# Performance work log

Hardware: AMD Instinct MI355X
Metric: run time of the kernel (lower is better)

## Reference

```python
import jax, jax.numpy as jnp
import numpy as np

N_HEAD = 16

def setup_inputs() -> dict:
    key = jax.random.key(0)
    ks = jax.random.split(key, 5)
    C = 1024
    s = 1.0 / np.sqrt(C)
    x = jax.random.normal(ks[0], (2, 2048, C), dtype=jnp.float32)
    wq = jax.random.normal(ks[1], (C, C), dtype=jnp.float32) * s
    wk = jax.random.normal(ks[2], (C, C), dtype=jnp.float32) * s
    wv = jax.random.normal(ks[3], (C, C), dtype=jnp.float32) * s
    wp = jax.random.normal(ks[4], (C, C), dtype=jnp.float32) * s
    z = jnp.zeros((C,), dtype=jnp.float32)
    return {"x": x, "wq": wq, "bq": z, "wk": wk, "bk": z,
            "wv": wv, "bv": z, "wp": wp, "bp": z}

def reference(x, wq, bq, wk, bk, wv, bv, wp, bp):
    B, T, C = x.shape
    H = N_HEAD
    D = C // H
    # projections: weights stored as (in, out) -> x @ w + b
    q = (x @ wq + bq).reshape(B, T, H, D).transpose(0, 2, 1, 3)  # [B,H,T,D]
    k = (x @ wk + bk).reshape(B, T, H, D).transpose(0, 2, 1, 3)
    v = (x @ wv + bv).reshape(B, T, H, D).transpose(0, 2, 1, 3)
    att = jnp.einsum('bhqd,bhkd->bhqk', q, k) / jnp.sqrt(jnp.float32(D))
    causal = jnp.tril(jnp.ones((T, T), dtype=bool))
    att = jnp.where(causal[None, None], att, -jnp.inf)
    att = jax.nn.softmax(att, axis=-1)
    out = jnp.einsum('bhqk,bhkd->bhqd', att, v)  # [B,H,T,D]
    out = out.transpose(0, 2, 1, 3).reshape(B, T, C)
    return out @ wp + bp
```

## Files before the change

### kernel.cpp

```cpp
#include <hip/hip_runtime.h>
#include <hip/hip_bf16.h>
#include <stdint.h>


typedef __attribute__((ext_vector_type(8)))  short bf16x8;
typedef __attribute__((ext_vector_type(4)))  float f32x4;
typedef __attribute__((ext_vector_type(16))) float f32x16;
typedef __attribute__((ext_vector_type(4)))  short short4v;

#define MFMA16(a,b,c) __builtin_amdgcn_mfma_f32_16x16x32_bf16(a,b,c,0,0,0)
#define MFMA32(a,b,c) __builtin_amdgcn_mfma_f32_32x32x16_bf16(a,b,c,0,0,0)

__device__ __forceinline__ unsigned short f2bfu(float f){
  union { __hip_bfloat16 h; unsigned short u; } cv;
  cv.h = __float2bfloat16(f);
  return cv.u;
}
__device__ __forceinline__ float bfu2f(unsigned u){
  union { unsigned v; float f; } cv;
  cv.v = u << 16;
  return cv.f;
}

__device__ __forceinline__ unsigned cvtpk(float a, float b){
  unsigned r;
  asm("v_cvt_pk_bf16_f32 %0, %1, %2" : "=v"(r) : "v"(a), "v"(b));
  return r;
}

__device__ __forceinline__ void permswap(unsigned &x, unsigned &y){
  asm volatile("v_permlane32_swap_b32 %0, %1" : "+v"(x), "+v"(y));
}

__device__ __forceinline__ void async16(const void* g, void* s){
  __builtin_amdgcn_global_load_lds((const __attribute__((address_space(1))) void*)g,
                                   (__attribute__((address_space(3))) void*)s, 16, 0, 0);
}

__global__ __launch_bounds__(256)
void prep_k(const float* __restrict__ x, unsigned short* __restrict__ xb,
            const float* __restrict__ wq, const float* __restrict__ wk,
            const float* __restrict__ wv, const float* __restrict__ wp,
            unsigned short* __restrict__ wqkvT, unsigned short* __restrict__ wpT)
{
  __shared__ float t[32][33];
  const int bx = blockIdx.x;
  const int tid = threadIdx.x;
  if (bx < 4096) {
    const int i = bx * 256 + tid;
    const float4 v = ((const float4*)x)[i];
    short4v o;
    o.x = (short)f2bfu(v.x); o.y = (short)f2bfu(v.y);
    o.z = (short)f2bfu(v.z); o.w = (short)f2bfu(v.w);
    ((short4v*)xb)[i] = o;
    return;
  }
  const int b = bx - 4096;
  const int wsel = b >> 10;
  const float* W = (wsel == 0) ? wq : (wsel == 1) ? wk : (wsel == 2) ? wv : wp;
  unsigned short* Wt = (wsel == 3) ? wpT : wqkvT + (size_t)wsel * 1024 * 1024;
  const int bc = ((b & 1023) & 31) * 32;
  const int br = ((b & 1023) >> 5) * 32;
  const int tx = tid & 31, ty = tid >> 5;
  #pragma unroll
  for (int i = 0; i < 32; i += 8)
    t[ty + i][tx] = W[(size_t)(br + ty + i) * 1024 + bc + tx];
  __syncthreads();
  #pragma unroll
  for (int i = 0; i < 32; i += 8)
    Wt[(size_t)(bc + ty + i) * 1024 + br + tx] = f2bfu(t[tx][ty + i]);
}

__global__ __launch_bounds__(256)
void gemm_qkv(const unsigned short* __restrict__ A, const unsigned short* __restrict__ Bt,
              const float* __restrict__ b0, const float* __restrict__ b1, const float* __restrict__ b2,
              unsigned short* __restrict__ Qo, unsigned short* __restrict__ Ko,
              unsigned short* __restrict__ Vo)
{
  constexpr int K = 1024;
  __shared__ unsigned short As[2][128 * 32];
  __shared__ unsigned short Bs[2][128 * 32];
  const int tid = threadIdx.x;
  const int lane = tid & 63;
  const int w = tid >> 6;
  const int l15 = lane & 15, lhi = lane >> 4;
  const int row0 = blockIdx.y * 128;
  const int col0 = blockIdx.x * 128;
  const int wr = (w >> 1) * 64;
  const int wc = (w & 1) * 64;

  f32x4 acc[4][4];
  #pragma unroll
  for (int i = 0; i < 4; i++)
    #pragma unroll
    for (int j = 0; j < 4; j++) acc[i][j] = 0.0f;

  const int srow = lane >> 2;
  const int scol = (lane & 3) * 8;
  const unsigned short* Ab = A  + (size_t)(row0 + w * 32 + srow) * K + scol;
  const unsigned short* Bb = Bt + (size_t)(col0 + w * 32 + srow) * K + scol;
  const int wofs = (w * 32) * 32;

  auto stageg = [&](int k0, int buf) {
    async16(Ab + k0,          &As[buf][wofs]);
    async16(Ab + k0 + 16 * K, &As[buf][wofs + 16 * 32]);
    async16(Bb + k0,          &Bs[buf][wofs]);
    async16(Bb + k0 + 16 * K, &Bs[buf][wofs + 16 * 32]);
  };

  stageg(0, 0);
  __syncthreads();
  int cur = 0;
  for (int k0 = 0; k0 < K; k0 += 32) {
    if (k0 + 32 < K) stageg(k0 + 32, cur ^ 1);
    bf16x8 af[4], bfv[4];
    #pragma unroll
    for (int i = 0; i < 4; i++) {
      af[i]  = *(const bf16x8*)&As[cur][(wr + i * 16 + l15) * 32 + lhi * 8];
      bfv[i] = *(const bf16x8*)&Bs[cur][(wc + i * 16 + l15) * 32 + lhi * 8];
    }
    __builtin_amdgcn_s_setprio(1);
    #pragma unroll
    for (int i = 0; i < 4; i++)
      #pragma unroll
      for (int j = 0; j < 4; j++)
        acc[i][j] = MFMA16(af[i], bfv[j], acc[i][j]);
    __builtin_amdgcn_s_setprio(0);
    __syncthreads();
    cur ^= 1;
  }

  #pragma unroll
  for (int j = 0; j < 4; j++) {
    const int n = col0 + wc + j * 16 + l15;
    const int which = n >> 10;
    const int cn = n & 1023;
    const float bias = (which == 0 ? b0[cn] : which == 1 ? b1[cn] : b2[cn]);
    const int h = cn >> 6, d = cn & 63;
    if (which == 2) {
      #pragma unroll
      for (int i = 0; i < 4; i++) {
        const int m = row0 + wr + i * 16 + lhi * 4;
        const int b_ = m >> 11, t = m & 2047;
        uint2 pk;
        pk.x = cvtpk(acc[i][j][0] + bias, acc[i][j][1] + bias);
        pk.y = cvtpk(acc[i][j][2] + bias, acc[i][j][3] + bias);
        *(uint2*)(Vo + (((size_t)(b_ * 16 + h) * 64 + d) * 2048 + t)) = pk;
      }
    } else {
      unsigned short* dst = (which == 0 ? Qo : Ko);
      const float sc = (which == 0 ? 0.125f * 1.44269504f : 1.0f);
      #pragma unroll
      for (int i = 0; i < 4; i++)
        #pragma unroll
        for (int r = 0; r < 4; r++) {
          const int m = row0 + wr + i * 16 + lhi * 4 + r;
          const int b_ = m >> 11, t = m & 2047;
          dst[(((size_t)(b_ * 16 + h) * 2048 + t) * 64) + d] =
              f2bfu((acc[i][j][r] + bias) * sc);
        }
    }
  }
}

__global__ __launch_bounds__(256)
void gemm_proj(const unsigned short* __restrict__ A, const unsigned short* __restrict__ Bt,
               const float* __restrict__ bias_, float* __restrict__ Fo)
{
  constexpr int K = 1024;
  __shared__ unsigned short As[2][64 * 32];
  __shared__ unsigned short Bs[2][128 * 32];
  const int tid = threadIdx.x;
  const int lane = tid & 63;
  const int w = tid >> 6;
  const int l15 = lane & 15, lhi = lane >> 4;
  const int row0 = blockIdx.y * 64;
  const int col0 = blockIdx.x * 128;
  const int wr = (w >> 1) * 32;
  const int wc = (w & 1) * 64;

  f32x4 acc[2][4];
  #pragma unroll
  for (int i = 0; i < 2; i++)
    #pragma unroll
    for (int j = 0; j < 4; j++) acc[i][j] = 0.0f;

  const int srow = lane >> 2;
  const int scol = (lane & 3) * 8;
  const unsigned short* Ab = A  + (size_t)(row0 + w * 16 + srow) * K + scol;
  const unsigned short* Bb = Bt + (size_t)(col0 + w * 32 + srow) * K + scol;
  const int wofsA = (w * 16) * 32;
  const int wofsB = (w * 32) * 32;

  auto stageg = [&](int k0, int buf) {
    async16(Ab + k0,          &As[buf][wofsA]);
    async16(Bb + k0,          &Bs[buf][wofsB]);
    async16(Bb + k0 + 16 * K, &Bs[buf][wofsB + 16 * 32]);
  };

  stageg(0, 0);
  __syncthreads();
  int cur = 0;
  for (int k0 = 0; k0 < K; k0 += 32) {
    if (k0 + 32 < K) stageg(k0 + 32, cur ^ 1);
    bf16x8 af[2], bfv[4];
    #pragma unroll
    for (int i = 0; i < 2; i++)
      af[i]  = *(const bf16x8*)&As[cur][(wr + i * 16 + l15) * 32 + lhi * 8];
    #pragma unroll
    for (int j = 0; j < 4; j++)
      bfv[j] = *(const bf16x8*)&Bs[cur][(wc + j * 16 + l15) * 32 + lhi * 8];
    __builtin_amdgcn_s_setprio(1);
    #pragma unroll
    for (int i = 0; i < 2; i++)
      #pragma unroll
      for (int j = 0; j < 4; j++)
        acc[i][j] = MFMA16(af[i], bfv[j], acc[i][j]);
    __builtin_amdgcn_s_setprio(0);
    __syncthreads();
    cur ^= 1;
  }

  #pragma unroll
  for (int j = 0; j < 4; j++) {
    const int n = col0 + wc + j * 16 + l15;
    const float bias = bias_[n];
    #pragma unroll
    for (int i = 0; i < 2; i++)
      #pragma unroll
      for (int r = 0; r < 4; r++) {
        const int m = row0 + wr + i * 16 + lhi * 4 + r;
        Fo[(size_t)m * 1024 + n] = acc[i][j][r] + bias;
      }
  }
}


__global__ __launch_bounds__(256)
void attn_k(const unsigned short* __restrict__ Q, const unsigned short* __restrict__ Kg,
            const unsigned short* __restrict__ VT,
            unsigned short* __restrict__ Op0, unsigned short* __restrict__ Op1,
            float* __restrict__ ml0, float* __restrict__ ml1)
{
  __shared__ unsigned short Ks[2][64 * 64];
  __shared__ unsigned short Vs[2][64 * 64];
  const int flat = blockIdx.y * 8 + blockIdx.x;
  const int u = (flat & 7) * 32 + (flat >> 3);
  const int bx = u & 7, bh = u >> 3;
  const int e = blockIdx.z;
  const int tid = threadIdx.x, lane = tid & 63, w = tid >> 6;
  const int r0 = lane & 31, hi5 = lane >> 5;
  const int p  = bx * 4 + w;
  const int pB = 63 - p;
  const int q0A = p * 32, q0B = pB * 32;
  const int jmA = p >> 1, jmB = pB >> 1;
  const int jmax = (63 - bx * 4) >> 1;

  unsigned short* Op = e ? Op1 : Op0;
  float* ml = e ? ml1 : ml0;

  const unsigned short* Kbh  = Kg + (size_t)bh * (2048 * 64);
  const unsigned short* VTbh = VT + (size_t)bh * (64 * 2048);

  bf16x8 qfA[4], qfB[4];
  {
    const unsigned short* QA = Q + ((size_t)bh * 2048 + q0A + r0) * 64 + hi5 * 8;
    const unsigned short* QB = Q + ((size_t)bh * 2048 + q0B + r0) * 64 + hi5 * 8;
    #pragma unroll
    for (int s = 0; s < 4; s++) {
      qfA[s] = *(const bf16x8*)(QA + s * 16);
      qfB[s] = *(const bf16x8*)(QB + s * 16);
    }
  }

  f32x16 oA[2], oB[2];
  #pragma unroll
  for (int d = 0; d < 2; d++) { oA[d] = 0.0f; oB[d] = 0.0f; }
  float mA = -1e30f, lA = 0.0f, mB = -1e30f, lB = 0.0f;

  int fragoff[4];
  #pragma unroll
  for (int t = 0; t < 4; t++)
    fragoff[t] = (r0 * 128 + t * 32 + hi5 * 16) ^ ((r0 & 7) << 4);

  const int srow = w * 8 + (lane >> 3);
  const int cole = (((lane & 7) ^ (lane >> 3)) << 3);
  const unsigned short* Ksrc = Kbh + (size_t)srow * 64 + cole;
  const unsigned short* Vsrc = VTbh + (size_t)srow * 2048 + cole;

  auto stage = [&](int kv0, int buf) {
    unsigned short* kb = &Ks[buf][w * 512];
    unsigned short* vb = &Vs[buf][w * 512];
    #pragma unroll
    for (int it = 0; it < 2; ++it) {
      async16(Ksrc + (size_t)(kv0 + it * 32) * 64, kb + it * 2048);
      async16(Vsrc + (size_t)(it * 32) * 2048 + kv0, vb + it * 2048);
    }
  };

  const unsigned short* Ksb;
  const unsigned short* Vsb;

  auto member = [&](f32x16 (&oT)[2], const bf16x8 (&qf)[4],
                    float& mrun, float& lrun, int q0, int kv0, bool mask) {
    f32x16 s0 = 0.0f, s1 = 0.0f;
    __builtin_amdgcn_s_setprio(1);
    #pragma unroll
    for (int t = 0; t < 4; t++) {
      const bf16x8 ka = *(const bf16x8*)((const char*)Ksb + fragoff[t]);
      const bf16x8 kb = *(const bf16x8*)((const char*)Ksb + fragoff[t] + 4096);
      s0 = MFMA32(ka, qf[t], s0);
      s1 = MFMA32(kb, qf[t], s1);
    }
    __builtin_amdgcn_s_setprio(0);

    const int q = q0 + r0;
    if (mask) {
      #pragma unroll
      for (int r = 0; r < 16; r++) {
        const int kvr = kv0 + (r & 3) + 8 * (r >> 2) + 4 * hi5;
        if (kvr      > q) s0[r] = -1e30f;
        if (kvr + 32 > q) s1[r] = -1e30f;
      }
    }

    float pm = fmaxf(s0[0], s1[0]);
    #pragma unroll
    for (int r = 1; r < 16; r++) pm = fmaxf(pm, fmaxf(s0[r], s1[r]));
    pm = fmaxf(pm, __shfl_xor(pm, 32, 64));

    if (__any((int)(pm > mrun + 8.0f))) {
      const float mnew = fmaxf(mrun, pm);
      const float sc = exp2f(mrun - mnew);
      mrun = mnew; lrun *= sc;
      oT[0] *= sc; oT[1] *= sc;
    }

    float p0[16], p1[16];
    float rs = 0.0f;
    #pragma unroll
    for (int r = 0; r < 16; r++) {
      p0[r] = exp2f(s0[r] - mrun);
      p1[r] = exp2f(s1[r] - mrun);
      rs += p0[r] + p1[r];
    }
    rs += __shfl_xor(rs, 32, 64);
    lrun += rs;

    bf16x8 pb[4];
    #pragma unroll
    for (int sub = 0; sub < 2; sub++) {
      {
        unsigned a = cvtpk(p0[sub*8+0], p0[sub*8+1]);
        unsigned b = cvtpk(p0[sub*8+2], p0[sub*8+3]);
        unsigned c = cvtpk(p0[sub*8+4], p0[sub*8+5]);
        unsigned d = cvtpk(p0[sub*8+6], p0[sub*8+7]);
        permswap(a, c); permswap(b, d);
        union { unsigned u[4]; bf16x8 hv; } wv_;
        wv_.u[0] = a; wv_.u[1] = b; wv_.u[2] = c; wv_.u[3] = d;
        pb[sub] = wv_.hv;
      }
      {
        unsigned a = cvtpk(p1[sub*8+0], p1[sub*8+1]);
        unsigned b = cvtpk(p1[sub*8+2], p1[sub*8+3]);
        unsigned c = cvtpk(p1[sub*8+4], p1[sub*8+5]);
        unsigned d = cvtpk(p1[sub*8+6], p1[sub*8+7]);
        permswap(a, c); permswap(b, d);
        union { unsigned u[4]; bf16x8 hv; } wv_;
        wv_.u[0] = a; wv_.u[1] = b; wv_.u[2] = c; wv_.u[3] = d;
        pb[2 + sub] = wv_.hv;
      }
    }

    __builtin_amdgcn_s_setprio(1);
    #pragma unroll
    for (int t = 0; t < 4; t++) {
      const bf16x8 va = *(const bf16x8*)((const char*)Vsb + fragoff[t]);
      const bf16x8 vb = *(const bf16x8*)((const char*)Vsb + fragoff[t] + 4096);
      oT[0] = MFMA32(va, pb[t], oT[0]);
      oT[1] = MFMA32(vb, pb[t], oT[1]);
    }
    __builtin_amdgcn_s_setprio(0);
  };

  stage(e * 64, 0);
  __syncthreads();

  int cur = 0;
  for (int t = e; t <= jmax; t += 2) {
    if (t + 2 <= jmax) stage((t + 2) * 64, cur ^ 1);
    Ksb = &Ks[cur][0];
    Vsb = &Vs[cur][0];
    const int kv0 = t * 64;
    if (t <= jmB) member(oB, qfB, mB, lB, q0B, kv0, t == jmB);
    if (t <= jmA) member(oA, qfA, mA, lA, q0A, kv0, t == jmA);
    __syncthreads();
    cur ^= 1;
  }

  auto emitp = [&](f32x16 (&oT)[2], float m, float l, int p_) {
    const float inv = (l > 0.0f) ? 1.0f / l : 0.0f;
    const size_t rbase = (size_t)(bh * 64 + p_) * 32 + r0;
    if (hi5 == 0) {
      float2 v; v.x = m; v.y = l;
      *(float2*)(ml + rbase * 2) = v;
    }
    unsigned short* base = Op + rbase * 64 + hi5 * 4;
    #pragma unroll
    for (int dh = 0; dh < 2; dh++)
      #pragma unroll
      for (int g = 0; g < 4; g++) {
        uint2 pk;
        pk.x = cvtpk(oT[dh][4*g]   * inv, oT[dh][4*g+1] * inv);
        pk.y = cvtpk(oT[dh][4*g+2] * inv, oT[dh][4*g+3] * inv);
        *(uint2*)(base + dh * 32 + g * 8) = pk;
      }
  };
  emitp(oA, mA, lA, p);
  emitp(oB, mB, lB, pB);
}

__global__ __launch_bounds__(256)
void combine_k(const unsigned short* __restrict__ O0, const unsigned short* __restrict__ O1,
               const float* __restrict__ ml0, const float* __restrict__ ml1,
               unsigned short* __restrict__ Ob)
{
  const int g = blockIdx.x;
  const int bh = g >> 6, p = g & 63;
  const int b_ = bh >> 4, h = bh & 15;
  const int tid = threadIdx.x;
  const int row = tid >> 3, c8 = (tid & 7) * 8;
  const size_t rbase = (size_t)g * 32 + row;
  const float2 v0 = *(const float2*)(ml0 + rbase * 2);
  const float2 v1 = *(const float2*)(ml1 + rbase * 2);
  const float mm = fmaxf(v0.x, v1.x);
  const float w0 = v0.y * exp2f(v0.x - mm);
  const float w1 = v1.y * exp2f(v1.x - mm);
  const float inv = 1.0f / (w0 + w1);
  const float a0 = w0 * inv, a1 = w1 * inv;
  const uint4 u0 = *(const uint4*)(O0 + rbase * 64 + c8);
  const uint4 u1 = *(const uint4*)(O1 + rbase * 64 + c8);
  uint4 o;
  o.x = cvtpk(a0 * bfu2f(u0.x & 0xffffu) + a1 * bfu2f(u1.x & 0xffffu),
              a0 * bfu2f(u0.x >> 16)     + a1 * bfu2f(u1.x >> 16));
  o.y = cvtpk(a0 * bfu2f(u0.y & 0xffffu) + a1 * bfu2f(u1.y & 0xffffu),
              a0 * bfu2f(u0.y >> 16)     + a1 * bfu2f(u1.y >> 16));
  o.z = cvtpk(a0 * bfu2f(u0.z & 0xffffu) + a1 * bfu2f(u1.z & 0xffffu),
              a0 * bfu2f(u0.z >> 16)     + a1 * bfu2f(u1.z >> 16));
  o.w = cvtpk(a0 * bfu2f(u0.w & 0xffffu) + a1 * bfu2f(u1.w & 0xffffu),
              a0 * bfu2f(u0.w >> 16)     + a1 * bfu2f(u1.w >> 16));
  unsigned short* dst = Ob + ((size_t)b_ * 2048 + p * 32 + row) * 1024 + h * 64 + c8;
  *(uint4*)dst = o;
}


extern "C" void kernel_launch(void* const* d_in, const int* in_sizes, int n_in,
                              void* d_out, int out_size, void* d_ws, size_t ws_size,
                              hipStream_t stream) {
  const float* x  = (const float*)d_in[0];
  const float* wq = (const float*)d_in[1];
  const float* bq = (const float*)d_in[2];
  const float* wk = (const float*)d_in[3];
  const float* bk = (const float*)d_in[4];
  const float* wv = (const float*)d_in[5];
  const float* bv = (const float*)d_in[6];
  const float* wp = (const float*)d_in[7];
  const float* bp = (const float*)d_in[8];
  float* out = (float*)d_out;

  char* ws = (char*)d_ws;
  const size_t MB = 1024 * 1024;
  unsigned short* xb    = (unsigned short*)(ws);
  unsigned short* wqkvT = (unsigned short*)(ws + 8  * MB);
  unsigned short* wpT   = (unsigned short*)(ws + 14 * MB);
  unsigned short* Qb    = (unsigned short*)(ws + 16 * MB);
  unsigned short* Kb    = (unsigned short*)(ws + 24 * MB);
  unsigned short* VTb   = (unsigned short*)(ws + 32 * MB);
  unsigned short* Op0   = (unsigned short*)(ws);
  float*          ml0   = (float*)(ws + 8 * MB);
  float*          ml1   = (float*)(ws + 8 * MB + 512 * 1024);
  unsigned short* Op1   = (unsigned short*)d_out;
  unsigned short* Ob    = Qb;

  prep_k<<<dim3(8192), dim3(256), 0, stream>>>(x, xb, wq, wk, wv, wp, wqkvT, wpT);

  gemm_qkv<<<dim3(24, 32), dim3(256), 0, stream>>>(xb, wqkvT, bq, bk, bv,
                                                   Qb, Kb, VTb);
  attn_k<<<dim3(8, 32, 2), dim3(256), 0, stream>>>(Qb, Kb, VTb, Op0, Op1, ml0, ml1);
  combine_k<<<dim3(2048), dim3(256), 0, stream>>>(Op0, Op1, ml0, ml1, Ob);
  gemm_proj<<<dim3(8, 64), dim3(256), 0, stream>>>(Ob, wpT, bp, out);
}
```

Measured before the change: 122.7 us.

## Fuse split-KV attention combine into output projection GEMM A-tile load

```diff
diff --git a/kernel.cpp b/kernel.cpp
--- a/kernel.cpp
+++ b/kernel.cpp
@@ -235,6 +235,115 @@
   }
 }
 
+__global__ __launch_bounds__(256)
+void gemm_projf(const unsigned short* __restrict__ O0, const unsigned short* __restrict__ O1,
+                const float* __restrict__ ml0, const float* __restrict__ ml1,
+                const unsigned short* __restrict__ Bt,
+                const float* __restrict__ bias_, float* __restrict__ Fo)
+{
+  constexpr int K = 1024;
+  __shared__ unsigned short As[2][64 * 32];
+  __shared__ unsigned short Bs[2][128 * 32];
+  const int tid = threadIdx.x;
+  const int lane = tid & 63;
+  const int w = tid >> 6;
+  const int l15 = lane & 15, lhi = lane >> 4;
+  const int row0 = blockIdx.y * 64;
+  const int col0 = blockIdx.x * 128;
+  const int wr = (w >> 1) * 32;
+  const int wc = (w & 1) * 64;
+
+  f32x4 acc[2][4];
+  #pragma unroll
+  for (int i = 0; i < 2; i++)
+    #pragma unroll
+    for (int j = 0; j < 4; j++) acc[i][j] = 0.0f;
+
+  const int srow = lane >> 2;
+  const int scol = (lane & 3) * 8;
+  const int arow = row0 + w * 16 + srow;
+  const int b_ = arow >> 11, tr = arow & 2047;
+  const int pt = tr >> 5, rr = tr & 31;
+  const size_t rb_base = ((size_t)(b_ * 16) * 64 + pt) * 32 + rr;
+
+  const unsigned short* Bb = Bt + (size_t)(col0 + w * 32 + srow) * K + scol;
+  const int wofsB = (w * 32) * 32;
+  unsigned short* AsW0 = &As[0][(w * 16 + srow) * 32 + scol];
+  unsigned short* AsW1 = &As[1][(w * 16 + srow) * 32 + scol];
+
+  auto stageB = [&](int k0, int buf) {
+    async16(Bb + k0,          &Bs[buf][wofsB]);
+    async16(Bb + k0 + 16 * K, &Bs[buf][wofsB + 16 * 32]);
+  };
+
+  uint4 u0, u1;
+  float aw0, aw1;
+  auto loadA = [&](int k0) {
+    const int h = k0 >> 6;
+    const size_t rbase = rb_base + (size_t)h * 2048;
+    const float2 v0 = *(const float2*)(ml0 + rbase * 2);
+    const float2 v1 = *(const float2*)(ml1 + rbase * 2);
+    const float mm = fmaxf(v0.x, v1.x);
+    const float w0_ = v0.y * exp2f(v0.x - mm);
+    const float w1_ = v1.y * exp2f(v1.x - mm);
+    const float inv = 1.0f / (w0_ + w1_);
+    aw0 = w0_ * inv; aw1 = w1_ * inv;
+    const int d0 = (k0 & 63) + scol;
+    u0 = *(const uint4*)(O0 + rbase * 64 + d0);
+    u1 = *(const uint4*)(O1 + rbase * 64 + d0);
+  };
+  auto writeA = [&](int buf) {
+    uint4 o;
+    o.x = cvtpk(aw0 * bfu2f(u0.x & 0xffffu) + aw1 * bfu2f(u1.x & 0xffffu),
+                aw0 * bfu2f(u0.x >> 16)     + aw1 * bfu2f(u1.x >> 16));
+    o.y = cvtpk(aw0 * bfu2f(u0.y & 0xffffu) + aw1 * bfu2f(u1.y & 0xffffu),
+                aw0 * bfu2f(u0.y >> 16)     + aw1 * bfu2f(u1.y >> 16));
+    o.z = cvtpk(aw0 * bfu2f(u0.z & 0xffffu) + aw1 * bfu2f(u1.z & 0xffffu),
+                aw0 * bfu2f(u0.z >> 16)     + aw1 * bfu2f(u1.z >> 16));
+    o.w = cvtpk(aw0 * bfu2f(u0.w & 0xffffu) + aw1 * bfu2f(u1.w & 0xffffu),
+                aw0 * bfu2f(u0.w >> 16)     + aw1 * bfu2f(u1.w >> 16));
+    *(uint4*)(buf ? AsW1 : AsW0) = o;
+  };
+
+  loadA(0);
+  stageB(0, 0);
+  writeA(0);
+  __syncthreads();
+  int cur = 0;
+  for (int k0 = 0; k0 < K; k0 += 32) {
+    if (k0 + 32 < K) { stageB(k0 + 32, cur ^ 1); loadA(k0 + 32); }
+    bf16x8 af[2], bfv[4];
+    #pragma unroll
+    for (int i = 0; i < 2; i++)
+      af[i]  = *(const bf16x8*)&As[cur][(wr + i * 16 + l15) * 32 + lhi * 8];
+    #pragma unroll
+    for (int j = 0; j < 4; j++)
+      bfv[j] = *(const bf16x8*)&Bs[cur][(wc + j * 16 + l15) * 32 + lhi * 8];
+    __builtin_amdgcn_s_setprio(1);
+    #pragma unroll
+    for (int i = 0; i < 2; i++)
+      #pragma unroll
+      for (int j = 0; j < 4; j++)
+        acc[i][j] = MFMA16(af[i], bfv[j], acc[i][j]);
+    __builtin_amdgcn_s_setprio(0);
+    if (k0 + 32 < K) writeA(cur ^ 1);
+    __syncthreads();
+    cur ^= 1;
+  }
+
+  #pragma unroll
+  for (int j = 0; j < 4; j++) {
+    const int n = col0 + wc + j * 16 + l15;
+    const float bias = bias_[n];
+    #pragma unroll
+    for (int i = 0; i < 2; i++)
+      #pragma unroll
+      for (int r = 0; r < 4; r++) {
+        const int m = row0 + wr + i * 16 + lhi * 4 + r;
+        Fo[(size_t)m * 1024 + n] = acc[i][j][r] + bias;
+      }
+  }
+}
 
 __global__ __launch_bounds__(256)
 void attn_k(const unsigned short* __restrict__ Q, const unsigned short* __restrict__ Kg,
@@ -479,14 +588,22 @@
   unsigned short* Op0   = (unsigned short*)(ws);
   float*          ml0   = (float*)(ws + 8 * MB);
   float*          ml1   = (float*)(ws + 8 * MB + 512 * 1024);
-  unsigned short* Op1   = (unsigned short*)d_out;
-  unsigned short* Ob    = Qb;
+
+  const bool bigws = (ws_size >= 48 * MB);
+  unsigned short* Op1 = bigws ? (unsigned short*)(ws + 40 * MB)
+                              : (unsigned short*)d_out;
+  unsigned short* Ob  = Qb;
 
   prep_k<<<dim3(8192), dim3(256), 0, stream>>>(x, xb, wq, wk, wv, wp, wqkvT, wpT);
 
   gemm_qkv<<<dim3(24, 32), dim3(256), 0, stream>>>(xb, wqkvT, bq, bk, bv,
                                                    Qb, Kb, VTb);
   attn_k<<<dim3(8, 32, 2), dim3(256), 0, stream>>>(Qb, Kb, VTb, Op0, Op1, ml0, ml1);
-  combine_k<<<dim3(2048), dim3(256), 0, stream>>>(Op0, Op1, ml0, ml1, Ob);
-  gemm_proj<<<dim3(8, 64), dim3(256), 0, stream>>>(Ob, wpT, bp, out);
-}
+  if (bigws) {
+    gemm_projf<<<dim3(8, 64), dim3(256), 0, stream>>>(Op0, Op1, ml0, ml1,
+                                                      wpT, bp, out);
+  } else {
+    combine_k<<<dim3(2048), dim3(256), 0, stream>>>(Op0, Op1, ml0, ml1, Ob);
+    gemm_proj<<<dim3(8, 64), dim3(256), 0, stream>>>(Ob, wpT, bp, out);
+  }
+}
```

After: 129.9 us. +5.9%, slower.
